# Kernel optimization log

Hardware: AMD Instinct MI355X
Metric: run time of the kernel (lower is better)

Reference implementation:

```python
import jax, jax.numpy as jnp
import numpy as np
from jax import lax

DN = ('NCHW', 'OIHW', 'NCHW')

def _attn(x, w):
    # x: [B, C, H, W]; channel pool -> [B, 2, H, W]
    pool = jnp.concatenate([x.max(axis=1, keepdims=True), x.mean(axis=1, keepdims=True)], axis=1)
    g = lax.conv_general_dilated(pool, w, (1, 1), [(3, 3), (3, 3)], dimension_numbers=DN)
    return x * jax.nn.sigmoid(g)

def setup_inputs() -> dict:
    key = jax.random.key(0)
    k0, k1, k2, k3, k4 = jax.random.split(key, 5)
    B, C, H, W = 16, 128, 32, 512
    x = jax.random.normal(k0, (B, C, H, W), dtype=jnp.float32)
    wg = jax.random.normal(k1, (C, C // 2, 1, 3), dtype=jnp.float32) * 0.05  # groups=2 conv weight
    w1 = jax.random.normal(k2, (1, 2, 7, 7), dtype=jnp.float32) * 0.1
    w2 = jax.random.normal(k3, (1, 2, 7, 7), dtype=jnp.float32) * 0.1
    w3 = jax.random.normal(k4, (1, 2, 7, 7), dtype=jnp.float32) * 0.1
    return {"x": x, "wg": wg, "w1": w1, "w2": w2, "w3": w3}

def reference(x, wg, w1, w2, w3):
    # grouped (1,3) conv, padding (0,1), groups=2, no bias
    x = lax.conv_general_dilated(x, wg, (1, 1), [(0, 0), (1, 1)],
                                 dimension_numbers=DN, feature_group_count=2)
    o1 = _attn(x, w1)
    o2 = jnp.transpose(_attn(jnp.transpose(x, (0, 2, 1, 3)), w2), (0, 2, 1, 3))
    o3 = jnp.transpose(_attn(jnp.transpose(x, (0, 3, 2, 1)), w3), (0, 3, 2, 1))
    return (o1 + o2 + o3) / 3.0
```

## Files before the change

### kernel.cpp

```cpp
#include <hip/hip_runtime.h>
#include <math.h>

#define B 16
#define C 128
#define H 32
#define W 512

typedef short bf16x4 __attribute__((ext_vector_type(4)));
typedef short bf16x8 __attribute__((ext_vector_type(8)));
typedef float f32x4 __attribute__((ext_vector_type(4)));

static __device__ inline unsigned short f2bf(float f) {
    unsigned u = __builtin_bit_cast(unsigned, f);
    u += 0x7fffu + ((u >> 16) & 1u);
    return (unsigned short)(u >> 16);
}
static __device__ inline unsigned pack2(float a, float b) {
    unsigned u;
    asm("v_cvt_pk_bf16_f32 %0, %1, %2" : "=v"(u) : "v"(a), "v"(b));
    return u;
}
static __device__ inline float bflo(unsigned u) {
    return __builtin_bit_cast(float, u << 16);
}
static __device__ inline float bfhi(unsigned u) {
    return __builtin_bit_cast(float, u & 0xffff0000u);
}

__global__ __launch_bounds__(256) void prep_wT(const float* __restrict__ wg,
                                               unsigned short* __restrict__ wT) {
    const int e = blockIdx.x * 256 + threadIdx.x;
    if (e >= 24576) return;
    const int g   = e / 12288;
    const int rem = e - g * 12288;
    const int tap = rem >> 12;
    const int o   = (rem >> 6) & 63;
    const int ci  = rem & 63;
    wT[e] = f2bf(wg[((size_t)(g * 64 + o) * 64 + ci) * 3 + tap]);
}

__global__ __launch_bounds__(256) void conv_pools(
    const float* __restrict__ x, const unsigned short* __restrict__ wT,
    unsigned* __restrict__ pool3p, unsigned* __restrict__ pool1p,
    unsigned* __restrict__ pool2p) {
    __shared__ __align__(16) char xsb[2][34 * 144];
    __shared__ __align__(16) float ytile[2][32][68];

    const int bx = blockIdx.x;
    const int f  = bx & 31;
    const int g  = f & 1;
    const int b  = f >> 1;
    const int chunk = bx >> 5;
    const int wq = chunk >> 1;
    const int hq = chunk & 1;
    const int h0 = hq * 16;
    const int t  = threadIdx.x;
    const int lane = t & 63;
    const int col  = lane & 15;
    const int q    = lane >> 4;
    const int wave = t >> 6;

    const unsigned short* wA =
        wT + (size_t)g * 12288 + wave * 1024 + col * 64 + q * 8;
    bf16x8 wfr[3][2];
#pragma unroll
    for (int tap = 0; tap < 3; ++tap)
#pragma unroll
        for (int kk = 0; kk < 2; ++kk)
            wfr[tap][kk] = *(const bf16x8*)(wA + tap * 4096 + kk * 32);

    float a[2][4];
    float hv = 0.f;
    const int w0l = (t & 7) * 4;
    const int ci0 = (t >> 3) * 2;
    const float* xb0 = x + (size_t)(b * C + g * 64 + ci0) * (H * W) + wq * 32 + w0l;
    const int side = (t >> 6) & 1;
    const int hci  = t & 63;
    const int gw   = wq * 32 + (side ? 32 : -1);
    const bool hvalid = (t < 128) && (side ? (wq < 15) : (wq > 0));
    const float* xh0 = x + (size_t)(b * C + g * 64 + hci) * (H * W) + gw;

    auto LOADX = [&](int h) {
        const float4 v0 = *(const float4*)(xb0 + h * W);
        const float4 v1 = *(const float4*)(xb0 + (size_t)(H * W) + h * W);
        a[0][0] = v0.x; a[0][1] = v0.y; a[0][2] = v0.z; a[0][3] = v0.w;
        a[1][0] = v1.x; a[1][1] = v1.y; a[1][2] = v1.z; a[1][3] = v1.w;
        hv = hvalid ? xh0[h * W] : 0.f;
    };
    auto WRITEX = [&](char* buf) {
#pragma unroll
        for (int j = 0; j < 4; ++j)
            *(unsigned*)(buf + (size_t)(w0l + j + 1) * 144 + ci0 * 2) =
                pack2(a[0][j], a[1][j]);
        if (t < 128)
            *(unsigned short*)(buf + (size_t)(side ? 33 : 0) * 144 + hci * 2) = f2bf(hv);
    };

    f32x4 mH[2], sH[2];
#pragma unroll
    for (int wt = 0; wt < 2; ++wt) {
        mH[wt] = (f32x4){-INFINITY, -INFINITY, -INFINITY, -INFINITY};
        sH[wt] = (f32x4){0.f, 0.f, 0.f, 0.f};
    }

    const int wl = t >> 3;
    const int e  = t & 7;

    LOADX(h0);
    WRITEX(xsb[0]);
    LOADX(h0 + 1);
    __syncthreads();

    for (int hh = 0; hh < 16; ++hh) {
        const int h   = h0 + hh;
        const int cur = hh & 1;

        f32x4 acc[2];
        acc[0] = (f32x4){0.f, 0.f, 0.f, 0.f};
        acc[1] = (f32x4){0.f, 0.f, 0.f, 0.f};
        {
            const char* ab = xsb[cur] + q * 16;
#pragma unroll
            for (int wt = 0; wt < 2; ++wt)
#pragma unroll
                for (int kk = 0; kk < 2; ++kk)
#pragma unroll
                    for (int tap = 0; tap < 3; ++tap) {
                        const bf16x8 xf = *(const bf16x8*)(
                            ab + (size_t)(wt * 16 + col + tap) * 144 + kk * 64);
                        acc[wt] = __builtin_amdgcn_mfma_f32_16x16x32_bf16(
                            xf, wfr[tap][kk], acc[wt], 0, 0, 0);
                    }
        }

#pragma unroll
        for (int wt = 0; wt < 2; ++wt)
#pragma unroll
            for (int r = 0; r < 4; ++r) {
                mH[wt][r] = fmaxf(mH[wt][r], acc[wt][r]);
                sH[wt][r] += acc[wt][r];
            }

        {
            float m = acc[0][0], s = acc[0][0];
            m = fmaxf(fmaxf(m, acc[0][1]), fmaxf(acc[0][2], acc[0][3]));
            s += acc[0][1] + acc[0][2] + acc[0][3];
#pragma unroll
            for (int r = 0; r < 4; ++r) {
                m = fmaxf(m, acc[1][r]);
                s += acc[1][r];
            }
            m = fmaxf(m, __shfl_xor(m, 16)); s += __shfl_xor(s, 16);
            m = fmaxf(m, __shfl_xor(m, 32)); s += __shfl_xor(s, 32);
            if (lane < 16)
                pool3p[((size_t)(wq * B + b) * H + h) * C + g * 64 + wave * 16 + lane] =
                    pack2(m, s);
        }

#pragma unroll
        for (int wt = 0; wt < 2; ++wt)
#pragma unroll
            for (int r = 0; r < 4; ++r)
                ytile[cur][wt * 16 + q * 4 + r][wave * 16 + col] = acc[wt][r];

        if (hh < 15) WRITEX(xsb[cur ^ 1]);
        if (hh < 14) LOADX(h + 2);
        __syncthreads();

        {
            const f32x4 v0 = *(const f32x4*)&ytile[cur][wl][e * 8];
            const f32x4 v1 = *(const f32x4*)&ytile[cur][wl][e * 8 + 4];
            float m = fmaxf(fmaxf(v0[0], v0[1]), fmaxf(v0[2], v0[3]));
            float s = v0[0] + v0[1] + v0[2] + v0[3];
            m = fmaxf(m, fmaxf(fmaxf(v1[0], v1[1]), fmaxf(v1[2], v1[3])));
            s += v1[0] + v1[1] + v1[2] + v1[3];
#pragma unroll
            for (int off = 1; off <= 4; off <<= 1) {
                m = fmaxf(m, __shfl_xor(m, off));
                s += __shfl_xor(s, off);
            }
            if (e == 0)
                pool1p[((size_t)(g * B + b) * H + h) * W + wq * 32 + wl] = pack2(m, s);
        }
    }

    {
        const int o = g * 64 + wave * 16 + col;
        unsigned* p2 = pool2p + ((size_t)(hq * B + b) * C + o) * W + wq * 32 + q * 4;
#pragma unroll
        for (int wt = 0; wt < 2; ++wt) {
            uint4 pk;
            pk.x = pack2(mH[wt][0], sH[wt][0]);
            pk.y = pack2(mH[wt][1], sH[wt][1]);
            pk.z = pack2(mH[wt][2], sH[wt][2]);
            pk.w = pack2(mH[wt][3], sH[wt][3]);
            *(uint4*)(p2 + wt * 16) = pk;
        }
    }
}

__global__ __launch_bounds__(256) void conv_apply(
    const float* __restrict__ x, const unsigned short* __restrict__ wT,
    const float* __restrict__ s1, const float* __restrict__ s2,
    const float* __restrict__ s3, float* __restrict__ out) {
    __shared__ __align__(16) char xsb[2][34 * 144];

    const int bx = blockIdx.x;
    const int f  = bx & 31;
    const int g  = f & 1;
    const int b  = f >> 1;
    const int chunk = bx >> 5;
    const int wq = chunk >> 2;
    const int hq = chunk & 3;
    const int h0 = hq * 8;
    const int t  = threadIdx.x;
    const int lane = t & 63;
    const int col  = lane & 15;
    const int q    = lane >> 4;
    const int wave = t >> 6;

    const unsigned short* wA =
        wT + (size_t)g * 12288 + wave * 1024 + col * 64 + q * 8;
    bf16x8 wfr[3][2];
#pragma unroll
    for (int tap = 0; tap < 3; ++tap)
#pragma unroll
        for (int kk = 0; kk < 2; ++kk)
            wfr[tap][kk] = *(const bf16x8*)(wA + tap * 4096 + kk * 32);

    float a[2][4];
    float hv = 0.f;
    const int w0l = (t & 7) * 4;
    const int ci0 = (t >> 3) * 2;
    const float* xb0 = x + (size_t)(b * C + g * 64 + ci0) * (H * W) + wq * 32 + w0l;
    const int side = (t >> 6) & 1;
    const int hci  = t & 63;
    const int gw   = wq * 32 + (side ? 32 : -1);
    const bool hvalid = (t < 128) && (side ? (wq < 15) : (wq > 0));
    const float* xh0 = x + (size_t)(b * C + g * 64 + hci) * (H * W) + gw;

    auto LOADX = [&](int h) {
        const float4 v0 = *(const float4*)(xb0 + h * W);
        const float4 v1 = *(const float4*)(xb0 + (size_t)(H * W) + h * W);
        a[0][0] = v0.x; a[0][1] = v0.y; a[0][2] = v0.z; a[0][3] = v0.w;
        a[1][0] = v1.x; a[1][1] = v1.y; a[1][2] = v1.z; a[1][3] = v1.w;
        hv = hvalid ? xh0[h * W] : 0.f;
    };
    auto WRITEX = [&](char* buf) {
#pragma unroll
        for (int j = 0; j < 4; ++j)
            *(unsigned*)(buf + (size_t)(w0l + j + 1) * 144 + ci0 * 2) =
                pack2(a[0][j], a[1][j]);
        if (t < 128)
            *(unsigned short*)(buf + (size_t)(side ? 33 : 0) * 144 + hci * 2) = f2bf(hv);
    };

    const int o = g * 64 + wave * 16 + col;
    const float4 g2a = *(const float4*)(s2 + ((size_t)b * C + o) * W + wq * 32 + q * 4);
    const float4 g2b = *(const float4*)(s2 + ((size_t)b * C + o) * W + wq * 32 + q * 4 + 16);

    LOADX(h0);
    WRITEX(xsb[0]);
    LOADX(h0 + 1);
    __syncthreads();

    for (int hh = 0; hh < 8; ++hh) {
        const int h   = h0 + hh;
        const int cur = hh & 1;

        f32x4 acc[2];
        acc[0] = (f32x4){0.f, 0.f, 0.f, 0.f};
        acc[1] = (f32x4){0.f, 0.f, 0.f, 0.f};
        {
            const char* ab = xsb[cur] + q * 16;
#pragma unroll
            for (int wt = 0; wt < 2; ++wt)
#pragma unroll
                for (int kk = 0; kk < 2; ++kk)
#pragma unroll
                    for (int tap = 0; tap < 3; ++tap) {
                        const bf16x8 xf = *(const bf16x8*)(
                            ab + (size_t)(wt * 16 + col + tap) * 144 + kk * 64);
                        acc[wt] = __builtin_amdgcn_mfma_f32_16x16x32_bf16(
                            xf, wfr[tap][kk], acc[wt], 0, 0, 0);
                    }
        }

        const float4 g1a = *(const float4*)(s1 + ((size_t)b * H + h) * W + wq * 32 + q * 4);
        const float4 g1b = *(const float4*)(s1 + ((size_t)b * H + h) * W + wq * 32 + q * 4 + 16);
        const float  g3v = s3[((size_t)b * H + h) * C + o];
        const float  k   = 1.f / 3.f;

        float* ob = out + ((size_t)(b * C + o) * H + h) * W + wq * 32 + q * 4;
        f32x4 o0, o1;
        o0[0] = acc[0][0] * (g1a.x + g2a.x + g3v) * k;
        o0[1] = acc[0][1] * (g1a.y + g2a.y + g3v) * k;
        o0[2] = acc[0][2] * (g1a.z + g2a.z + g3v) * k;
        o0[3] = acc[0][3] * (g1a.w + g2a.w + g3v) * k;
        o1[0] = acc[1][0] * (g1b.x + g2b.x + g3v) * k;
        o1[1] = acc[1][1] * (g1b.y + g2b.y + g3v) * k;
        o1[2] = acc[1][2] * (g1b.z + g2b.z + g3v) * k;
        o1[3] = acc[1][3] * (g1b.w + g2b.w + g3v) * k;
        *(f32x4*)ob        = o0;
        *(f32x4*)(ob + 16) = o1;

        if (hh < 7) WRITEX(xsb[cur ^ 1]);
        if (hh < 6) LOADX(h + 2);
        __syncthreads();
    }
}

__global__ __launch_bounds__(256) void combine(const unsigned* __restrict__ p1p,
                                               const unsigned* __restrict__ p3p,
                                               unsigned* __restrict__ p2p,
                                               float* __restrict__ pool1,
                                               float* __restrict__ pool3) {
    const int bid = blockIdx.x;
    if (bid < 256) {
        const int n = bid * 256 + threadIdx.x;
        const int idx4 = n * 4;
        const uint4 u0 = *(const uint4*)(p1p + idx4);
        const uint4 u1 = *(const uint4*)(p1p + 262144 + idx4);
        const int b = idx4 >> 14;
        const int o = idx4 & 16383;
        float4 m, s;
        const float k = 1.f / C;
        m.x = fmaxf(bflo(u0.x), bflo(u1.x)); s.x = (bfhi(u0.x) + bfhi(u1.x)) * k;
        m.y = fmaxf(bflo(u0.y), bflo(u1.y)); s.y = (bfhi(u0.y) + bfhi(u1.y)) * k;
        m.z = fmaxf(bflo(u0.z), bflo(u1.z)); s.z = (bfhi(u0.z) + bfhi(u1.z)) * k;
        m.w = fmaxf(bflo(u0.w), bflo(u1.w)); s.w = (bfhi(u0.w) + bfhi(u1.w)) * k;
        *(float4*)(pool1 + ((size_t)(b * 2 + 0) * H * W) + o) = m;
        *(float4*)(pool1 + ((size_t)(b * 2 + 1) * H * W) + o) = s;
    } else if (bid < 512) {
        const int n = (bid - 256) * 256 + threadIdx.x;
        const int b = n >> 12;
        const int o = n & 4095;
        float m = -INFINITY, s = 0.f;
#pragma unroll
        for (int wq = 0; wq < 16; ++wq) {
            const unsigned u = p3p[(size_t)(wq * B + b) * 4096 + o];
            m = fmaxf(m, bflo(u));
            s += bfhi(u);
        }
        pool3[((size_t)(b * 2 + 0) * H * C) + o] = m;
        pool3[((size_t)(b * 2 + 1) * H * C) + o] = s * (1.f / W);
    } else {
        const int n = (bid - 512) * 256 + threadIdx.x;
        const int idx4 = n * 4;
        const uint4 u0 = *(const uint4*)(p2p + idx4);
        const uint4 u1 = *(const uint4*)(p2p + 1048576 + idx4);
        const float k = 1.f / H;
        uint4 r;
        r.x = pack2(fmaxf(bflo(u0.x), bflo(u1.x)), (bfhi(u0.x) + bfhi(u1.x)) * k);
        r.y = pack2(fmaxf(bflo(u0.y), bflo(u1.y)), (bfhi(u0.y) + bfhi(u1.y)) * k);
        r.z = pack2(fmaxf(bflo(u0.z), bflo(u1.z)), (bfhi(u0.z) + bfhi(u1.z)) * k);
        r.w = pack2(fmaxf(bflo(u0.w), bflo(u1.w)), (bfhi(u0.w) + bfhi(u1.w)) * k);
        *(uint4*)(p2p + idx4) = r;
    }
}

__global__ __launch_bounds__(256) void gates(
    const float* __restrict__ pool1, const unsigned* __restrict__ pool2,
    const float* __restrict__ pool3, const float* __restrict__ w1,
    const float* __restrict__ w2, const float* __restrict__ w3,
    float* __restrict__ s1, float* __restrict__ s2, float* __restrict__ s3) {
    const int bid = blockIdx.x;
    if (bid >= 256 && bid < 1280) {
        const int n  = (bid - 256) * 256 + threadIdx.x;
        const int q0 = (n & 127) * 4;
        const int p  = (n >> 7) & 127;
        const int b  = n >> 14;
        float acc0 = 0.f, acc1 = 0.f, acc2 = 0.f, acc3 = 0.f;
#pragma unroll
        for (int i = 0; i < 7; ++i) {
            const int pp = p + i - 3;
            if (pp < 0 || pp >= C) continue;
            const unsigned* row = pool2 + ((size_t)b * C + pp) * W;
            unsigned win[10];
#pragma unroll
            for (int j = 0; j < 10; ++j) {
                const int qq = q0 + j - 3;
                win[j] = (qq >= 0 && qq < W) ? row[qq] : 0u;
            }
            const float* wr0 = w2 + i * 7;
            const float* wr1 = w2 + 49 + i * 7;
#pragma unroll
            for (int j = 0; j < 7; ++j) {
                const float wv0 = wr0[j], wv1 = wr1[j];
                acc0 += bflo(win[j])     * wv0 + bfhi(win[j])     * wv1;
                acc1 += bflo(win[j + 1]) * wv0 + bfhi(win[j + 1]) * wv1;
                acc2 += bflo(win[j + 2]) * wv0 + bfhi(win[j + 2]) * wv1;
                acc3 += bflo(win[j + 3]) * wv0 + bfhi(win[j + 3]) * wv1;
            }
        }
        float4 o;
        o.x = 1.f / (1.f + expf(-acc0));
        o.y = 1.f / (1.f + expf(-acc1));
        o.z = 1.f / (1.f + expf(-acc2));
        o.w = 1.f / (1.f + expf(-acc3));
        *(float4*)(s2 + (size_t)n * 4) = o;
        return;
    }
    const float* pin; const float* wgt; float* so; int P, Q, n;
    if (bid < 256) { pin = pool1; wgt = w1; so = s1; P = H; Q = W;
                     n = bid * 256 + threadIdx.x; }
    else           { pin = pool3; wgt = w3; so = s3; P = H; Q = C;
                     n = (bid - 1280) * 256 + threadIdx.x; }
    const int q4   = Q >> 2;
    const int q0   = (n % q4) * 4;
    const int rest = n / q4;
    const int p    = rest % P;
    const int b    = rest / P;
    float acc0 = 0.f, acc1 = 0.f, acc2 = 0.f, acc3 = 0.f;
#pragma unroll
    for (int c2 = 0; c2 < 2; ++c2) {
#pragma unroll
        for (int i = 0; i < 7; ++i) {
            const int pp = p + i - 3;
            if (pp < 0 || pp >= P) continue;
            const float* row = pin + ((size_t)(b * 2 + c2) * P + pp) * Q;
            float win[10];
#pragma unroll
            for (int j = 0; j < 10; ++j) {
                const int qq = q0 + j - 3;
                win[j] = (qq >= 0 && qq < Q) ? row[qq] : 0.f;
            }
            const float* wr = wgt + c2 * 49 + i * 7;
#pragma unroll
            for (int j = 0; j < 7; ++j) {
                const float wv = wr[j];
                acc0 += win[j]     * wv;
                acc1 += win[j + 1] * wv;
                acc2 += win[j + 2] * wv;
                acc3 += win[j + 3] * wv;
            }
        }
    }
    float4 o;
    o.x = 1.f / (1.f + expf(-acc0));
    o.y = 1.f / (1.f + expf(-acc1));
    o.z = 1.f / (1.f + expf(-acc2));
    o.w = 1.f / (1.f + expf(-acc3));
    *(float4*)(so + (size_t)n * 4) = o;
}

extern "C" void kernel_launch(void* const* d_in, const int* in_sizes, int n_in,
                              void* d_out, int out_size, void* d_ws, size_t ws_size,
                              hipStream_t stream) {
    const float* x  = (const float*)d_in[0];
    const float* wg = (const float*)d_in[1];
    const float* w1 = (const float*)d_in[2];
    const float* w2 = (const float*)d_in[3];
    const float* w3 = (const float*)d_in[4];
    float* out = (float*)d_out;
    float* ws  = (float*)d_ws;

    unsigned* pool1p = (unsigned*)ws;
    unsigned* pool3p = (unsigned*)(ws + 524288);
    unsigned* pool2p = (unsigned*)(ws + 1572864);
    float* pool1 = ws + 3670016;
    float* pool3 = ws + 4194304;
    unsigned short* wT = (unsigned short*)(ws + 4325376);
    float* s1 = ws;
    float* s3 = ws + 262144;
    float* s2 = ws + 524288;

    prep_wT<<<dim3(96), 256, 0, stream>>>(wg, wT);
    conv_pools<<<dim3(1024), 256, 0, stream>>>(x, wT, pool3p, pool1p, pool2p);
    combine<<<dim3(1536), 256, 0, stream>>>(pool1p, pool3p, pool2p, pool1, pool3);
    gates<<<dim3(1344), 256, 0, stream>>>(pool1, pool2p, pool3, w1, w2, w3, s1, s2, s3);
    conv_apply<<<dim3(2048), 256, 0, stream>>>(x, wT, s1, s2, s3, out);
}
```

Before: 135.5 us.

## Deepen x prefetch to two rows and fold pool1/pool2 combine into gates

The conv kernels now keep two register buffers of x rows and issue global loads two steps ahead, unrolling the row loop by two so the load latency is hidden behind more MFMA work. The combine kernel shrinks to reducing only pool3. The max/sum merge of the two group halves for pool1 and the two H halves for pool2 moves into the gates kernel, which reads the packed bf16 partials directly. This removes a large intermediate write and read and most of the combine launch, at the cost of more registers and duplicated partial reads in gates.

```diff
diff --git a/kernel.cpp b/kernel.cpp
--- a/kernel.cpp
+++ b/kernel.cpp
@@ -69,8 +69,8 @@
         for (int kk = 0; kk < 2; ++kk)
             wfr[tap][kk] = *(const bf16x8*)(wA + tap * 4096 + kk * 32);
 
-    float a[2][4];
-    float hv = 0.f;
+    float a0[2][4], a1[2][4];
+    float hv0 = 0.f, hv1 = 0.f;
     const int w0l = (t & 7) * 4;
     const int ci0 = (t >> 3) * 2;
     const float* xb0 = x + (size_t)(b * C + g * 64 + ci0) * (H * W) + wq * 32 + w0l;
@@ -80,21 +80,23 @@
     const bool hvalid = (t < 128) && (side ? (wq < 15) : (wq > 0));
     const float* xh0 = x + (size_t)(b * C + g * 64 + hci) * (H * W) + gw;
 
-    auto LOADX = [&](int h) {
-        const float4 v0 = *(const float4*)(xb0 + h * W);
-        const float4 v1 = *(const float4*)(xb0 + (size_t)(H * W) + h * W);
-        a[0][0] = v0.x; a[0][1] = v0.y; a[0][2] = v0.z; a[0][3] = v0.w;
-        a[1][0] = v1.x; a[1][1] = v1.y; a[1][2] = v1.z; a[1][3] = v1.w;
-        hv = hvalid ? xh0[h * W] : 0.f;
-    };
-    auto WRITEX = [&](char* buf) {
-#pragma unroll
-        for (int j = 0; j < 4; ++j)
-            *(unsigned*)(buf + (size_t)(w0l + j + 1) * 144 + ci0 * 2) =
-                pack2(a[0][j], a[1][j]);
-        if (t < 128)
-            *(unsigned short*)(buf + (size_t)(side ? 33 : 0) * 144 + hci * 2) = f2bf(hv);
-    };
+#define P_LOADX(AA, HVV, h)                                                  \
+    {                                                                        \
+        const float4 v0 = *(const float4*)(xb0 + (h) * W);                   \
+        const float4 v1 = *(const float4*)(xb0 + (size_t)(H * W) + (h) * W); \
+        AA[0][0] = v0.x; AA[0][1] = v0.y; AA[0][2] = v0.z; AA[0][3] = v0.w;  \
+        AA[1][0] = v1.x; AA[1][1] = v1.y; AA[1][2] = v1.z; AA[1][3] = v1.w;  \
+        HVV = hvalid ? xh0[(h) * W] : 0.f;                                   \
+    }
+#define P_WRITEX(AA, HVV, buf)                                               \
+    {                                                                        \
+        _Pragma("unroll") for (int j = 0; j < 4; ++j)                        \
+            *(unsigned*)((buf) + (size_t)(w0l + j + 1) * 144 + ci0 * 2) =    \
+                pack2(AA[0][j], AA[1][j]);                                   \
+        if (t < 128)                                                         \
+            *(unsigned short*)((buf) + (size_t)(side ? 33 : 0) * 144 +       \
+                               hci * 2) = f2bf(HVV);                         \
+    }
 
     f32x4 mH[2], sH[2];
 #pragma unroll
@@ -106,83 +108,77 @@
     const int wl = t >> 3;
     const int e  = t & 7;
 
-    LOADX(h0);
-    WRITEX(xsb[0]);
-    LOADX(h0 + 1);
+    P_LOADX(a0, hv0, h0);
+    P_WRITEX(a0, hv0, xsb[0]);
+    P_LOADX(a1, hv1, h0 + 1);
+    P_LOADX(a0, hv0, h0 + 2);
     __syncthreads();
 
-    for (int hh = 0; hh < 16; ++hh) {
-        const int h   = h0 + hh;
-        const int cur = hh & 1;
-
-        f32x4 acc[2];
-        acc[0] = (f32x4){0.f, 0.f, 0.f, 0.f};
-        acc[1] = (f32x4){0.f, 0.f, 0.f, 0.f};
-        {
-            const char* ab = xsb[cur] + q * 16;
-#pragma unroll
-            for (int wt = 0; wt < 2; ++wt)
-#pragma unroll
-                for (int kk = 0; kk < 2; ++kk)
-#pragma unroll
-                    for (int tap = 0; tap < 3; ++tap) {
-                        const bf16x8 xf = *(const bf16x8*)(
-                            ab + (size_t)(wt * 16 + col + tap) * 144 + kk * 64);
-                        acc[wt] = __builtin_amdgcn_mfma_f32_16x16x32_bf16(
-                            xf, wfr[tap][kk], acc[wt], 0, 0, 0);
-                    }
-        }
-
-#pragma unroll
-        for (int wt = 0; wt < 2; ++wt)
-#pragma unroll
-            for (int r = 0; r < 4; ++r) {
-                mH[wt][r] = fmaxf(mH[wt][r], acc[wt][r]);
-                sH[wt][r] += acc[wt][r];
-            }
-
-        {
-            float m = acc[0][0], s = acc[0][0];
-            m = fmaxf(fmaxf(m, acc[0][1]), fmaxf(acc[0][2], acc[0][3]));
-            s += acc[0][1] + acc[0][2] + acc[0][3];
-#pragma unroll
-            for (int r = 0; r < 4; ++r) {
-                m = fmaxf(m, acc[1][r]);
-                s += acc[1][r];
-            }
-            m = fmaxf(m, __shfl_xor(m, 16)); s += __shfl_xor(s, 16);
-            m = fmaxf(m, __shfl_xor(m, 32)); s += __shfl_xor(s, 32);
-            if (lane < 16)
-                pool3p[((size_t)(wq * B + b) * H + h) * C + g * 64 + wave * 16 + lane] =
-                    pack2(m, s);
-        }
-
-#pragma unroll
-        for (int wt = 0; wt < 2; ++wt)
-#pragma unroll
-            for (int r = 0; r < 4; ++r)
-                ytile[cur][wt * 16 + q * 4 + r][wave * 16 + col] = acc[wt][r];
-
-        if (hh < 15) WRITEX(xsb[cur ^ 1]);
-        if (hh < 14) LOADX(h + 2);
-        __syncthreads();
-
-        {
-            const f32x4 v0 = *(const f32x4*)&ytile[cur][wl][e * 8];
-            const f32x4 v1 = *(const f32x4*)&ytile[cur][wl][e * 8 + 4];
-            float m = fmaxf(fmaxf(v0[0], v0[1]), fmaxf(v0[2], v0[3]));
-            float s = v0[0] + v0[1] + v0[2] + v0[3];
-            m = fmaxf(m, fmaxf(fmaxf(v1[0], v1[1]), fmaxf(v1[2], v1[3])));
-            s += v1[0] + v1[1] + v1[2] + v1[3];
-#pragma unroll
-            for (int off = 1; off <= 4; off <<= 1) {
-                m = fmaxf(m, __shfl_xor(m, off));
-                s += __shfl_xor(s, off);
-            }
-            if (e == 0)
-                pool1p[((size_t)(g * B + b) * H + h) * W + wq * 32 + wl] = pack2(m, s);
-        }
-    }
+#define P_STEP(hh, CUR, AW, HW, AL, HL)                                        \
+    {                                                                          \
+        const int h = h0 + (hh);                                               \
+        f32x4 acc[2];                                                          \
+        acc[0] = (f32x4){0.f, 0.f, 0.f, 0.f};                                  \
+        acc[1] = (f32x4){0.f, 0.f, 0.f, 0.f};                                  \
+        {                                                                      \
+            const char* ab = xsb[CUR] + q * 16;                                \
+            _Pragma("unroll") for (int wt = 0; wt < 2; ++wt)                   \
+                _Pragma("unroll") for (int kk = 0; kk < 2; ++kk)               \
+                    _Pragma("unroll") for (int tap = 0; tap < 3; ++tap) {      \
+                        const bf16x8 xf = *(const bf16x8*)(                    \
+                            ab + (size_t)(wt * 16 + col + tap) * 144 +         \
+                            kk * 64);                                          \
+                        acc[wt] = __builtin_amdgcn_mfma_f32_16x16x32_bf16(     \
+                            xf, wfr[tap][kk], acc[wt], 0, 0, 0);               \
+                    }                                                          \
+        }                                                                      \
+        _Pragma("unroll") for (int wt = 0; wt < 2; ++wt)                       \
+            _Pragma("unroll") for (int r = 0; r < 4; ++r) {                    \
+                mH[wt][r] = fmaxf(mH[wt][r], acc[wt][r]);                      \
+                sH[wt][r] += acc[wt][r];                                       \
+            }                                                                  \
+        {                                                                      \
+            float m = acc[0][0], s = acc[0][0];                                \
+            m = fmaxf(fmaxf(m, acc[0][1]), fmaxf(acc[0][2], acc[0][3]));       \
+            s += acc[0][1] + acc[0][2] + acc[0][3];                            \
+            _Pragma("unroll") for (int r = 0; r < 4; ++r) {                    \
+                m = fmaxf(m, acc[1][r]);                                       \
+                s += acc[1][r];                                                \
+            }                                                                  \
+            m = fmaxf(m, __shfl_xor(m, 16)); s += __shfl_xor(s, 16);           \
+            m = fmaxf(m, __shfl_xor(m, 32)); s += __shfl_xor(s, 32);           \
+            if (lane < 16)                                                     \
+                pool3p[((size_t)(wq * B + b) * H + h) * C + g * 64 +           \
+                       wave * 16 + lane] = pack2(m, s);                        \
+        }                                                                      \
+        _Pragma("unroll") for (int wt = 0; wt < 2; ++wt)                       \
+            _Pragma("unroll") for (int r = 0; r < 4; ++r)                      \
+                ytile[CUR][wt * 16 + q * 4 + r][wave * 16 + col] = acc[wt][r]; \
+        if ((hh) < 15) P_WRITEX(AW, HW, xsb[(CUR) ^ 1]);                       \
+        if ((hh) < 13) P_LOADX(AL, HL, h0 + (hh) + 3);                         \
+        __syncthreads();                                                       \
+        {                                                                      \
+            const f32x4 v0 = *(const f32x4*)&ytile[CUR][wl][e * 8];            \
+            const f32x4 v1 = *(const f32x4*)&ytile[CUR][wl][e * 8 + 4];        \
+            float m = fmaxf(fmaxf(v0[0], v0[1]), fmaxf(v0[2], v0[3]));         \
+            float s = v0[0] + v0[1] + v0[2] + v0[3];                           \
+            m = fmaxf(m, fmaxf(fmaxf(v1[0], v1[1]), fmaxf(v1[2], v1[3])));     \
+            s += v1[0] + v1[1] + v1[2] + v1[3];                                \
+            _Pragma("unroll") for (int off = 1; off <= 4; off <<= 1) {         \
+                m = fmaxf(m, __shfl_xor(m, off));                              \
+                s += __shfl_xor(s, off);                                       \
+            }                                                                  \
+            if (e == 0)                                                        \
+                pool1p[((size_t)(g * B + b) * H + h) * W + wq * 32 + wl] =     \
+                    pack2(m, s);                                               \
+        }                                                                      \
+    }
+
+    for (int hh = 0; hh < 16; hh += 2) {
+        P_STEP(hh,     0, a1, hv1, a1, hv1);
+        P_STEP(hh + 1, 1, a0, hv0, a0, hv0);
+    }
+#undef P_STEP
 
     {
         const int o = g * 64 + wave * 16 + col;
@@ -228,8 +224,8 @@
         for (int kk = 0; kk < 2; ++kk)
             wfr[tap][kk] = *(const bf16x8*)(wA + tap * 4096 + kk * 32);
 
-    float a[2][4];
-    float hv = 0.f;
+    float a0[2][4], a1[2][4];
+    float hv0 = 0.f, hv1 = 0.f;
     const int w0l = (t & 7) * 4;
     const int ci0 = (t >> 3) * 2;
     const float* xb0 = x + (size_t)(b * C + g * 64 + ci0) * (H * W) + wq * 32 + w0l;
@@ -239,133 +235,127 @@
     const bool hvalid = (t < 128) && (side ? (wq < 15) : (wq > 0));
     const float* xh0 = x + (size_t)(b * C + g * 64 + hci) * (H * W) + gw;
 
-    auto LOADX = [&](int h) {
-        const float4 v0 = *(const float4*)(xb0 + h * W);
-        const float4 v1 = *(const float4*)(xb0 + (size_t)(H * W) + h * W);
-        a[0][0] = v0.x; a[0][1] = v0.y; a[0][2] = v0.z; a[0][3] = v0.w;
-        a[1][0] = v1.x; a[1][1] = v1.y; a[1][2] = v1.z; a[1][3] = v1.w;
-        hv = hvalid ? xh0[h * W] : 0.f;
-    };
-    auto WRITEX = [&](char* buf) {
-#pragma unroll
-        for (int j = 0; j < 4; ++j)
-            *(unsigned*)(buf + (size_t)(w0l + j + 1) * 144 + ci0 * 2) =
-                pack2(a[0][j], a[1][j]);
-        if (t < 128)
-            *(unsigned short*)(buf + (size_t)(side ? 33 : 0) * 144 + hci * 2) = f2bf(hv);
-    };
-
     const int o = g * 64 + wave * 16 + col;
     const float4 g2a = *(const float4*)(s2 + ((size_t)b * C + o) * W + wq * 32 + q * 4);
     const float4 g2b = *(const float4*)(s2 + ((size_t)b * C + o) * W + wq * 32 + q * 4 + 16);
 
-    LOADX(h0);
-    WRITEX(xsb[0]);
-    LOADX(h0 + 1);
+    P_LOADX(a0, hv0, h0);
+    P_WRITEX(a0, hv0, xsb[0]);
+    P_LOADX(a1, hv1, h0 + 1);
+    P_LOADX(a0, hv0, h0 + 2);
     __syncthreads();
 
-    for (int hh = 0; hh < 8; ++hh) {
-        const int h   = h0 + hh;
-        const int cur = hh & 1;
-
-        f32x4 acc[2];
-        acc[0] = (f32x4){0.f, 0.f, 0.f, 0.f};
-        acc[1] = (f32x4){0.f, 0.f, 0.f, 0.f};
-        {
-            const char* ab = xsb[cur] + q * 16;
-#pragma unroll
-            for (int wt = 0; wt < 2; ++wt)
-#pragma unroll
-                for (int kk = 0; kk < 2; ++kk)
-#pragma unroll
-                    for (int tap = 0; tap < 3; ++tap) {
-                        const bf16x8 xf = *(const bf16x8*)(
-                            ab + (size_t)(wt * 16 + col + tap) * 144 + kk * 64);
-                        acc[wt] = __builtin_amdgcn_mfma_f32_16x16x32_bf16(
-                            xf, wfr[tap][kk], acc[wt], 0, 0, 0);
-                    }
-        }
-
-        const float4 g1a = *(const float4*)(s1 + ((size_t)b * H + h) * W + wq * 32 + q * 4);
-        const float4 g1b = *(const float4*)(s1 + ((size_t)b * H + h) * W + wq * 32 + q * 4 + 16);
-        const float  g3v = s3[((size_t)b * H + h) * C + o];
-        const float  k   = 1.f / 3.f;
-
-        float* ob = out + ((size_t)(b * C + o) * H + h) * W + wq * 32 + q * 4;
-        f32x4 o0, o1;
-        o0[0] = acc[0][0] * (g1a.x + g2a.x + g3v) * k;
-        o0[1] = acc[0][1] * (g1a.y + g2a.y + g3v) * k;
-        o0[2] = acc[0][2] * (g1a.z + g2a.z + g3v) * k;
-        o0[3] = acc[0][3] * (g1a.w + g2a.w + g3v) * k;
-        o1[0] = acc[1][0] * (g1b.x + g2b.x + g3v) * k;
-        o1[1] = acc[1][1] * (g1b.y + g2b.y + g3v) * k;
-        o1[2] = acc[1][2] * (g1b.z + g2b.z + g3v) * k;
-        o1[3] = acc[1][3] * (g1b.w + g2b.w + g3v) * k;
-        *(f32x4*)ob        = o0;
-        *(f32x4*)(ob + 16) = o1;
-
-        if (hh < 7) WRITEX(xsb[cur ^ 1]);
-        if (hh < 6) LOADX(h + 2);
-        __syncthreads();
-    }
-}
-
-__global__ __launch_bounds__(256) void combine(const unsigned* __restrict__ p1p,
-                                               const unsigned* __restrict__ p3p,
-                                               unsigned* __restrict__ p2p,
-                                               float* __restrict__ pool1,
+#define A_STEP(hh, CUR, AW, HW, AL, HL)                                        \
+    {                                                                          \
+        const int h = h0 + (hh);                                               \
+        f32x4 acc[2];                                                          \
+        acc[0] = (f32x4){0.f, 0.f, 0.f, 0.f};                                  \
+        acc[1] = (f32x4){0.f, 0.f, 0.f, 0.f};                                  \
+        {                                                                      \
+            const char* ab = xsb[CUR] + q * 16;                                \
+            _Pragma("unroll") for (int wt = 0; wt < 2; ++wt)                   \
+                _Pragma("unroll") for (int kk = 0; kk < 2; ++kk)               \
+                    _Pragma("unroll") for (int tap = 0; tap < 3; ++tap) {      \
+                        const bf16x8 xf = *(const bf16x8*)(                    \
+                            ab + (size_t)(wt * 16 + col + tap) * 144 +         \
+                            kk * 64);                                          \
+                        acc[wt] = __builtin_amdgcn_mfma_f32_16x16x32_bf16(     \
+                            xf, wfr[tap][kk], acc[wt], 0, 0, 0);               \
+                    }                                                          \
+        }                                                                      \
+        const float4 g1a =                                                     \
+            *(const float4*)(s1 + ((size_t)b * H + h) * W + wq * 32 + q * 4);  \
+        const float4 g1b = *(const float4*)(s1 + ((size_t)b * H + h) * W +     \
+                                            wq * 32 + q * 4 + 16);             \
+        const float g3v = s3[((size_t)b * H + h) * C + o];                     \
+        const float k   = 1.f / 3.f;                                           \
+        float* ob = out + ((size_t)(b * C + o) * H + h) * W + wq * 32 + q * 4; \
+        f32x4 o0, o1;                                                          \
+        o0[0] = acc[0][0] * (g1a.x + g2a.x + g3v) * k;                         \
+        o0[1] = acc[0][1] * (g1a.y + g2a.y + g3v) * k;                         \
+        o0[2] = acc[0][2] * (g1a.z + g2a.z + g3v) * k;                         \
+        o0[3] = acc[0][3] * (g1a.w + g2a.w + g3v) * k;                         \
+        o1[0] = acc[1][0] * (g1b.x + g2b.x + g3v) * k;                         \
+        o1[1] = acc[1][1] * (g1b.y + g2b.y + g3v) * k;                         \
+        o1[2] = acc[1][2] * (g1b.z + g2b.z + g3v) * k;                         \
+        o1[3] = acc[1][3] * (g1b.w + g2b.w + g3v) * k;                         \
+        *(f32x4*)ob        = o0;                                               \
+        *(f32x4*)(ob + 16) = o1;                                               \
+        if ((hh) < 7) P_WRITEX(AW, HW, xsb[(CUR) ^ 1]);                        \
+        if ((hh) < 5) P_LOADX(AL, HL, h0 + (hh) + 3);                          \
+        __syncthreads();                                                       \
+    }
+
+    for (int hh = 0; hh < 8; hh += 2) {
+        A_STEP(hh,     0, a1, hv1, a1, hv1);
+        A_STEP(hh + 1, 1, a0, hv0, a0, hv0);
+    }
+#undef A_STEP
+#undef P_LOADX
+#undef P_WRITEX
+}
+
+__global__ __launch_bounds__(256) void combine(const unsigned* __restrict__ p3p,
                                                float* __restrict__ pool3) {
-    const int bid = blockIdx.x;
-    if (bid < 256) {
-        const int n = bid * 256 + threadIdx.x;
-        const int idx4 = n * 4;
-        const uint4 u0 = *(const uint4*)(p1p + idx4);
-        const uint4 u1 = *(const uint4*)(p1p + 262144 + idx4);
-        const int b = idx4 >> 14;
-        const int o = idx4 & 16383;
-        float4 m, s;
-        const float k = 1.f / C;
-        m.x = fmaxf(bflo(u0.x), bflo(u1.x)); s.x = (bfhi(u0.x) + bfhi(u1.x)) * k;
-        m.y = fmaxf(bflo(u0.y), bflo(u1.y)); s.y = (bfhi(u0.y) + bfhi(u1.y)) * k;
-        m.z = fmaxf(bflo(u0.z), bflo(u1.z)); s.z = (bfhi(u0.z) + bfhi(u1.z)) * k;
-        m.w = fmaxf(bflo(u0.w), bflo(u1.w)); s.w = (bfhi(u0.w) + bfhi(u1.w)) * k;
-        *(float4*)(pool1 + ((size_t)(b * 2 + 0) * H * W) + o) = m;
-        *(float4*)(pool1 + ((size_t)(b * 2 + 1) * H * W) + o) = s;
-    } else if (bid < 512) {
-        const int n = (bid - 256) * 256 + threadIdx.x;
-        const int b = n >> 12;
-        const int o = n & 4095;
-        float m = -INFINITY, s = 0.f;
-#pragma unroll
-        for (int wq = 0; wq < 16; ++wq) {
-            const unsigned u = p3p[(size_t)(wq * B + b) * 4096 + o];
-            m = fmaxf(m, bflo(u));
-            s += bfhi(u);
-        }
-        pool3[((size_t)(b * 2 + 0) * H * C) + o] = m;
-        pool3[((size_t)(b * 2 + 1) * H * C) + o] = s * (1.f / W);
-    } else {
-        const int n = (bid - 512) * 256 + threadIdx.x;
-        const int idx4 = n * 4;
-        const uint4 u0 = *(const uint4*)(p2p + idx4);
-        const uint4 u1 = *(const uint4*)(p2p + 1048576 + idx4);
-        const float k = 1.f / H;
-        uint4 r;
-        r.x = pack2(fmaxf(bflo(u0.x), bflo(u1.x)), (bfhi(u0.x) + bfhi(u1.x)) * k);
-        r.y = pack2(fmaxf(bflo(u0.y), bflo(u1.y)), (bfhi(u0.y) + bfhi(u1.y)) * k);
-        r.z = pack2(fmaxf(bflo(u0.z), bflo(u1.z)), (bfhi(u0.z) + bfhi(u1.z)) * k);
-        r.w = pack2(fmaxf(bflo(u0.w), bflo(u1.w)), (bfhi(u0.w) + bfhi(u1.w)) * k);
-        *(uint4*)(p2p + idx4) = r;
-    }
+    const int n = blockIdx.x * 256 + threadIdx.x;
+    const int b = n >> 12;
+    const int o = n & 4095;
+    float m = -INFINITY, s = 0.f;
+#pragma unroll
+    for (int wq = 0; wq < 16; ++wq) {
+        const unsigned u = p3p[(size_t)(wq * B + b) * 4096 + o];
+        m = fmaxf(m, bflo(u));
+        s += bfhi(u);
+    }
+    pool3[((size_t)(b * 2 + 0) * H * C) + o] = m;
+    pool3[((size_t)(b * 2 + 1) * H * C) + o] = s * (1.f / W);
 }
 
 __global__ __launch_bounds__(256) void gates(
-    const float* __restrict__ pool1, const unsigned* __restrict__ pool2,
+    const unsigned* __restrict__ pool1p, const unsigned* __restrict__ pool2p,
     const float* __restrict__ pool3, const float* __restrict__ w1,
     const float* __restrict__ w2, const float* __restrict__ w3,
     float* __restrict__ s1, float* __restrict__ s2, float* __restrict__ s3) {
     const int bid = blockIdx.x;
-    if (bid >= 256 && bid < 1280) {
+    if (bid < 256) {
+        const int n  = bid * 256 + threadIdx.x;
+        const int q0 = (n & 127) * 4;
+        const int p  = (n >> 7) & 31;
+        const int b  = n >> 12;
+        float acc0 = 0.f, acc1 = 0.f, acc2 = 0.f, acc3 = 0.f;
+#pragma unroll
+        for (int i = 0; i < 7; ++i) {
+            const int pp = p + i - 3;
+            if (pp < 0 || pp >= H) continue;
+            const unsigned* r0 = pool1p + ((size_t)b * H + pp) * W;
+            const unsigned* r1 = r0 + 262144;
+            float vm[10], vs[10];
+#pragma unroll
+            for (int j = 0; j < 10; ++j) {
+                const int qq = q0 + j - 3;
+                const unsigned u0 = (qq >= 0 && qq < W) ? r0[qq] : 0u;
+                const unsigned u1 = (qq >= 0 && qq < W) ? r1[qq] : 0u;
+                vm[j] = fmaxf(bflo(u0), bflo(u1));
+                vs[j] = (bfhi(u0) + bfhi(u1)) * (1.f / C);
+            }
+            const float* wr0 = w1 + i * 7;
+            const float* wr1 = w1 + 49 + i * 7;
+#pragma unroll
+            for (int j = 0; j < 7; ++j) {
+                const float wv0 = wr0[j], wv1 = wr1[j];
+                acc0 += vm[j]     * wv0 + vs[j]     * wv1;
+                acc1 += vm[j + 1] * wv0 + vs[j + 1] * wv1;
+                acc2 += vm[j + 2] * wv0 + vs[j + 2] * wv1;
+                acc3 += vm[j + 3] * wv0 + vs[j + 3] * wv1;
+            }
+        }
+        float4 ov;
+        ov.x = 1.f / (1.f + expf(-acc0));
+        ov.y = 1.f / (1.f + expf(-acc1));
+        ov.z = 1.f / (1.f + expf(-acc2));
+        ov.w = 1.f / (1.f + expf(-acc3));
+        *(float4*)(s1 + (size_t)n * 4) = ov;
+    } else if (bid < 1280) {
         const int n  = (bid - 256) * 256 + threadIdx.x;
         const int q0 = (n & 127) * 4;
         const int p  = (n >> 7) & 127;
@@ -375,73 +365,71 @@
         for (int i = 0; i < 7; ++i) {
             const int pp = p + i - 3;
             if (pp < 0 || pp >= C) continue;
-            const unsigned* row = pool2 + ((size_t)b * C + pp) * W;
-            unsigned win[10];
+            const unsigned* r0 = pool2p + ((size_t)b * C + pp) * W;
+            const unsigned* r1 = r0 + 1048576;
+            float vm[10], vs[10];
 #pragma unroll
             for (int j = 0; j < 10; ++j) {
                 const int qq = q0 + j - 3;
-                win[j] = (qq >= 0 && qq < W) ? row[qq] : 0u;
+                const unsigned u0 = (qq >= 0 && qq < W) ? r0[qq] : 0u;
+                const unsigned u1 = (qq >= 0 && qq < W) ? r1[qq] : 0u;
+                vm[j] = fmaxf(bflo(u0), bflo(u1));
+                vs[j] = (bfhi(u0) + bfhi(u1)) * (1.f / H);
             }
             const float* wr0 = w2 + i * 7;
             const float* wr1 = w2 + 49 + i * 7;
 #pragma unroll
             for (int j = 0; j < 7; ++j) {
                 const float wv0 = wr0[j], wv1 = wr1[j];
-                acc0 += bflo(win[j])     * wv0 + bfhi(win[j])     * wv1;
-                acc1 += bflo(win[j + 1]) * wv0 + bfhi(win[j + 1]) * wv1;
-                acc2 += bflo(win[j + 2]) * wv0 + bfhi(win[j + 2]) * wv1;
-                acc3 += bflo(win[j + 3]) * wv0 + bfhi(win[j + 3]) * wv1;
+                acc0 += vm[j]     * wv0 + vs[j]     * wv1;
+                acc1 += vm[j + 1] * wv0 + vs[j + 1] * wv1;
+                acc2 += vm[j + 2] * wv0 + vs[j + 2] * wv1;
+                acc3 += vm[j + 3] * wv0 + vs[j + 3] * wv1;
             }
         }
-        float4 o;
-        o.x = 1.f / (1.f + expf(-acc0));
-        o.y = 1.f / (1.f + expf(-acc1));
-        o.z = 1.f / (1.f + expf(-acc2));
-        o.w = 1.f / (1.f + expf(-acc3));
-        *(float4*)(s2 + (size_t)n * 4) = o;
-        return;
-    }
-    const float* pin; const float* wgt; float* so; int P, Q, n;
-    if (bid < 256) { pin = pool1; wgt = w1; so = s1; P = H; Q = W;
-                     n = bid * 256 + threadIdx.x; }
-    else           { pin = pool3; wgt = w3; so = s3; P = H; Q = C;
-                     n = (bid - 1280) * 256 + threadIdx.x; }
-    const int q4   = Q >> 2;
-    const int q0   = (n % q4) * 4;
-    const int rest = n / q4;
-    const int p    = rest % P;
-    const int b    = rest / P;
-    float acc0 = 0.f, acc1 = 0.f, acc2 = 0.f, acc3 = 0.f;
-#pragma unroll
-    for (int c2 = 0; c2 < 2; ++c2) {
-#pragma unroll
-        for (int i = 0; i < 7; ++i) {
-            const int pp = p + i - 3;
-            if (pp < 0 || pp >= P) continue;
-            const float* row = pin + ((size_t)(b * 2 + c2) * P + pp) * Q;
-            float win[10];
-#pragma unroll
-            for (int j = 0; j < 10; ++j) {
-                const int qq = q0 + j - 3;
-                win[j] = (qq >= 0 && qq < Q) ? row[qq] : 0.f;
-            }
-            const float* wr = wgt + c2 * 49 + i * 7;
-#pragma unroll
-            for (int j = 0; j < 7; ++j) {
-                const float wv = wr[j];
-                acc0 += win[j]     * wv;
-                acc1 += win[j + 1] * wv;
-                acc2 += win[j + 2] * wv;
-                acc3 += win[j + 3] * wv;
+        float4 ov;
+        ov.x = 1.f / (1.f + expf(-acc0));
+        ov.y = 1.f / (1.f + expf(-acc1));
+        ov.z = 1.f / (1.f + expf(-acc2));
+        ov.w = 1.f / (1.f + expf(-acc3));
+        *(float4*)(s2 + (size_t)n * 4) = ov;
+    } else {
+        const int n  = (bid - 1280) * 256 + threadIdx.x;
+        const int q0 = (n & 31) * 4;
+        const int p  = (n >> 5) & 31;
+        const int b  = n >> 10;
+        float acc0 = 0.f, acc1 = 0.f, acc2 = 0.f, acc3 = 0.f;
+#pragma unroll
+        for (int c2 = 0; c2 < 2; ++c2) {
+#pragma unroll
+            for (int i = 0; i < 7; ++i) {
+                const int pp = p + i - 3;
+                if (pp < 0 || pp >= H) continue;
+                const float* row = pool3 + ((size_t)(b * 2 + c2) * H + pp) * C;
+                float win[10];
+#pragma unroll
+                for (int j = 0; j < 10; ++j) {
+                    const int qq = q0 + j - 3;
+                    win[j] = (qq >= 0 && qq < C) ? row[qq] : 0.f;
+                }
+                const float* wr = w3 + c2 * 49 + i * 7;
+#pragma unroll
+                for (int j = 0; j < 7; ++j) {
+                    const float wv = wr[j];
+                    acc0 += win[j]     * wv;
+                    acc1 += win[j + 1] * wv;
+                    acc2 += win[j + 2] * wv;
+                    acc3 += win[j + 3] * wv;
+                }
             }
         }
-    }
-    float4 o;
-    o.x = 1.f / (1.f + expf(-acc0));
-    o.y = 1.f / (1.f + expf(-acc1));
-    o.z = 1.f / (1.f + expf(-acc2));
-    o.w = 1.f / (1.f + expf(-acc3));
-    *(float4*)(so + (size_t)n * 4) = o;
+        float4 ov;
+        ov.x = 1.f / (1.f + expf(-acc0));
+        ov.y = 1.f / (1.f + expf(-acc1));
+        ov.z = 1.f / (1.f + expf(-acc2));
+        ov.w = 1.f / (1.f + expf(-acc3));
+        *(float4*)(s3 + (size_t)n * 4) = ov;
+    }
 }
 
 extern "C" void kernel_launch(void* const* d_in, const int* in_sizes, int n_in,
@@ -458,16 +446,15 @@
     unsigned* pool1p = (unsigned*)ws;
     unsigned* pool3p = (unsigned*)(ws + 524288);
     unsigned* pool2p = (unsigned*)(ws + 1572864);
-    float* pool1 = ws + 3670016;
-    float* pool3 = ws + 4194304;
-    unsigned short* wT = (unsigned short*)(ws + 4325376);
-    float* s1 = ws;
-    float* s3 = ws + 262144;
+    float* pool3 = ws + 3670016;
+    unsigned short* wT = (unsigned short*)(ws + 3801088);
+    float* s1 = ws + 3813376;
+    float* s3 = ws + 4075520;
     float* s2 = ws + 524288;
 
     prep_wT<<<dim3(96), 256, 0, stream>>>(wg, wT);
     conv_pools<<<dim3(1024), 256, 0, stream>>>(x, wT, pool3p, pool1p, pool2p);
-    combine<<<dim3(1536), 256, 0, stream>>>(pool1p, pool3p, pool2p, pool1, pool3);
-    gates<<<dim3(1344), 256, 0, stream>>>(pool1, pool2p, pool3, w1, w2, w3, s1, s2, s3);
+    combine<<<dim3(256), 256, 0, stream>>>(pool3p, pool3);
+    gates<<<dim3(1344), 256, 0, stream>>>(pool1p, pool2p, pool3, w1, w2, w3, s1, s2, s3);
     conv_apply<<<dim3(2048), 256, 0, stream>>>(x, wT, s1, s2, s3, out);
 }
```

New measurement: 137.0 us. No clear change (+1.1%).
